# Kernel tuning notes

Hardware: AMD Instinct MI355X
Metric: run time of the kernel (lower is better)

The kernel has to match this reference:

```python
import jax, jax.numpy as jnp
import numpy as np

D_MODEL = 1024
NUM_HEADS = 16
HEAD_DIM = D_MODEL // NUM_HEADS


def setup_inputs() -> dict:
    key = jax.random.key(0)
    k_x, k_wqkv, k_bqkv, k_wo, k_bo = jax.random.split(key, 5)
    bound_qkv = 1.0 / np.sqrt(D_MODEL)
    x = jax.random.normal(k_x, (2, 2048, D_MODEL), dtype=jnp.float32)
    # torch nn.Linear init: U(-1/sqrt(fan_in), 1/sqrt(fan_in))
    W_qkv = jax.random.uniform(k_wqkv, (D_MODEL, 3 * D_MODEL), jnp.float32, -bound_qkv, bound_qkv)
    b_qkv = jax.random.uniform(k_bqkv, (3 * D_MODEL,), jnp.float32, -bound_qkv, bound_qkv)
    W_out = jax.random.uniform(k_wo, (D_MODEL, D_MODEL), jnp.float32, -bound_qkv, bound_qkv)
    b_out = jax.random.uniform(k_bo, (D_MODEL,), jnp.float32, -bound_qkv, bound_qkv)
    return {"x": x, "W_qkv": W_qkv, "b_qkv": b_qkv, "W_out": W_out, "b_out": b_out}


def reference(x, W_qkv, b_qkv, W_out, b_out):
    B, T, C = x.shape
    H, Dh = NUM_HEADS, HEAD_DIM
    qkv = x @ W_qkv + b_qkv                      # [B,T,3C]
    q, k, v = jnp.split(qkv, 3, axis=-1)
    # [B,T,C] -> [B,H,T,Dh]
    def to_heads(t):
        return t.reshape(B, T, H, Dh).transpose(0, 2, 1, 3)
    q, k, v = to_heads(q), to_heads(k), to_heads(v)
    scale = 1.0 / np.sqrt(Dh).astype(np.float32)
    scores = jnp.einsum("bhqd,bhkd->bhqk", q, k) * scale   # [B,H,T,T]
    weights = jax.nn.softmax(scores, axis=-1)
    attn = jnp.einsum("bhqk,bhkd->bhqd", weights, v)        # [B,H,T,Dh]
    attn = attn.transpose(0, 2, 1, 3).reshape(B, T, C)
    return attn @ W_out + b_out
```

## Files before the change

kernel.cpp:

```cpp
#include <hip/hip_runtime.h>

typedef __bf16 bf16x8 __attribute__((ext_vector_type(8)));
typedef float f32x4 __attribute__((ext_vector_type(4)));
typedef float f32x16 __attribute__((ext_vector_type(16)));

#define MFMA16(a, b, c) __builtin_amdgcn_mfma_f32_16x16x32_bf16(a, b, c, 0, 0, 0)
#define MFMA32(a, b, c) __builtin_amdgcn_mfma_f32_32x32x16_bf16(a, b, c, 0, 0, 0)
#define GLDS16(g, l)                                                              \
  __builtin_amdgcn_global_load_lds((const __attribute__((address_space(1))) void*)(g), \
                                   (__attribute__((address_space(3))) void*)(l), 16, 0, 0)

static __device__ __forceinline__ unsigned cvt_pk_bf16(float lo, float hi) {
  unsigned r;
  asm("v_cvt_pk_bf16_f32 %0, %1, %2" : "=v"(r) : "v"(lo), "v"(hi));
  return r;
}
static __device__ __forceinline__ void permswap(unsigned& a, unsigned& b) {
  asm("v_permlane32_swap_b32 %0, %1" : "+v"(a), "+v"(b));
}

__global__ __launch_bounds__(256) void cvt_bf16_kernel(const float* __restrict__ in,
                                                       __bf16* __restrict__ out, int n4) {
  int i = blockIdx.x * 256 + threadIdx.x;
  if (i < n4) {
    float4 v = ((const float4*)in)[i];
    union { __bf16 b[4]; uint2 u; } t;
    t.b[0] = (__bf16)v.x; t.b[1] = (__bf16)v.y;
    t.b[2] = (__bf16)v.z; t.b[3] = (__bf16)v.w;
    ((uint2*)out)[i] = t.u;
  }
}

__global__ __launch_bounds__(256) void transpose_w_kernel(const float* __restrict__ Wq,
                                                          __bf16* __restrict__ WqT,
                                                          const float* __restrict__ Wo,
                                                          __bf16* __restrict__ WoT) {
  const int Kd = 1024;
  int bx = blockIdx.x;
  const float* W; __bf16* WT; int Nd, n0;
  if (bx < 96) { W = Wq; WT = WqT; Nd = 3072; n0 = bx * 32; }
  else         { W = Wo; WT = WoT; Nd = 1024; n0 = (bx - 96) * 32; }
  __shared__ float tile[32][33];
  int k0 = blockIdx.y * 32;
  int tid = threadIdx.x;
  int kk = tid >> 3, nn = (tid & 7) * 4;
  float4 v = *(const float4*)&W[(size_t)(k0 + kk) * Nd + n0 + nn];
  tile[kk][nn] = v.x; tile[kk][nn + 1] = v.y;
  tile[kk][nn + 2] = v.z; tile[kk][nn + 3] = v.w;
  __syncthreads();
  int n2 = tid >> 3, k2 = (tid & 7) * 4;
  union { __bf16 b[4]; uint2 u; } t;
  t.b[0] = (__bf16)tile[k2][n2];
  t.b[1] = (__bf16)tile[k2 + 1][n2];
  t.b[2] = (__bf16)tile[k2 + 2][n2];
  t.b[3] = (__bf16)tile[k2 + 3][n2];
  *(uint2*)&WT[(size_t)(n0 + n2) * Kd + k0 + k2] = t.u;
}

template <bool OUT_F32, int NT>
__global__ __launch_bounds__(256) void gemm_kernel(const __bf16* __restrict__ A,
                                                   const __bf16* __restrict__ BT,
                                                   const float* __restrict__ bias,
                                                   void* __restrict__ Cout, int N,
                                                   int qn, float qs) {
  const int K = 1024;
  const int NJ = NT / 32;
  __shared__ __align__(16) __bf16 As[128 * 32];
  __shared__ __align__(16) __bf16 Bs[NT * 32];
  int tid = threadIdx.x;
  int wave = tid >> 6, lane = tid & 63;
  int quad = lane >> 4, l16 = lane & 15;
  int m0 = blockIdx.x * 128, n0 = blockIdx.y * NT;
  int wm = (wave >> 1) * 64, wn = (wave & 1) * (NT / 2);

  int srow = tid >> 2, scol = (tid & 3) * 8;
  const __bf16* aptr = A + (size_t)(m0 + srow) * K + scol;
  const __bf16* bptr = BT + (size_t)(n0 + srow) * K + scol;
  __bf16* asl = &As[(size_t)wave * 512];
  __bf16* bsl = &Bs[(size_t)wave * 512];

  f32x4 acc[4][NJ] = {};
  for (int k0 = 0; k0 < K; k0 += 32) {
    GLDS16(aptr + k0, asl);
    GLDS16(aptr + (size_t)64 * K + k0, asl + 2048);
    GLDS16(bptr + k0, bsl);
    if (NT == 128) GLDS16(bptr + (size_t)64 * K + k0, bsl + 2048);
    __syncthreads();
    bf16x8 af[4], bf[NJ];
    for (int i = 0; i < 4; i++)
      af[i] = *(bf16x8*)&As[(wm + i * 16 + l16) * 32 + quad * 8];
    for (int j = 0; j < NJ; j++)
      bf[j] = *(bf16x8*)&Bs[(wn + j * 16 + l16) * 32 + quad * 8];
    for (int i = 0; i < 4; i++)
      for (int j = 0; j < NJ; j++)
        acc[i][j] = MFMA16(af[i], bf[j], acc[i][j]);
    __syncthreads();
  }
  for (int j = 0; j < NJ; j++) {
    int col = n0 + wn + j * 16 + l16;
    float bv = bias[col];
    float sc = (col < qn) ? qs : 1.0f;
    for (int i = 0; i < 4; i++) {
      int rowb = m0 + wm + i * 16 + quad * 4;
      for (int r = 0; r < 4; r++) {
        float v = (acc[i][j][r] + bv) * sc;
        if (OUT_F32)
          ((float*)Cout)[(size_t)(rowb + r) * N + col] = v;
        else
          ((__bf16*)Cout)[(size_t)(rowb + r) * N + col] = (__bf16)v;
      }
    }
  }
}

__global__ __launch_bounds__(256) void transpose_v_kernel(const __bf16* __restrict__ qkv,
                                                          __bf16* __restrict__ Vt) {
  const int T = 2048, C3 = 3072;
  __shared__ __align__(16) __bf16 tile[64][72];
  int t0 = blockIdx.x * 64;
  int h = blockIdx.y, b = blockIdx.z;
  int tid = threadIdx.x;
  int tt = tid >> 2, c = (tid & 3) * 16;
  const __bf16* src = qkv + (size_t)(b * T + t0 + tt) * C3 + 2048 + h * 64 + c;
  *(uint4*)&tile[tt][c] = *(const uint4*)src;
  *(uint4*)&tile[tt][c + 8] = *(const uint4*)(src + 8);
  __syncthreads();
  int dd = tid >> 2, t2 = (tid & 3) * 16;
  union { __bf16 b_[16]; uint4 u[2]; } o;
  for (int i = 0; i < 16; i++) o.b_[i] = tile[t2 + i][dd];
  __bf16* dst = Vt + ((size_t)(b * 16 + h) * 64 + dd) * T + t0 + t2;
  *(uint4*)dst = o.u[0];
  *(uint4*)(dst + 8) = o.u[1];
}

struct AttnState {
  const char* lbase;
  char* wdst;
  int dK, dV;
  int lb[2][4];
};

template <int KRD, int VRD, int KST, int VST, bool DO_KST>
__device__ __forceinline__ void attn_iter(const AttnState& st, const __bf16* kg,
                                          const __bf16* vg, const bf16x8 (&qf)[4],
                                          const f32x16* sIN, f32x16* sOUT, f32x16& o0,
                                          f32x16& o1, float& rs) {
  __syncthreads();
  if constexpr (DO_KST) {
    GLDS16(kg, st.wdst + KST);
    GLDS16(kg + st.dK, st.wdst + KST + 4096);
  }
  GLDS16(vg, st.wdst + VST);
  GLDS16(vg + st.dV, st.wdst + VST + 4096);

  bf16x8 kf[2][4], vf[2][4];
#pragma unroll
  for (int rb = 0; rb < 2; rb++)
#pragma unroll
    for (int ds = 0; ds < 4; ds++)
      kf[rb][ds] = *(const bf16x8*)(st.lbase + st.lb[rb][ds] + KRD);
#pragma unroll
  for (int db = 0; db < 2; db++)
#pragma unroll
    for (int k2 = 0; k2 < 4; k2++)
      vf[db][k2] = *(const bf16x8*)(st.lbase + st.lb[db][k2] + VRD);

  f32x16 s0 = {}, s1 = {};
#pragma unroll
  for (int ds = 0; ds < 4; ds++) {
    s0 = MFMA32(kf[0][ds], qf[ds], s0);
    s1 = MFMA32(kf[1][ds], qf[ds], s1);
  }
  sOUT[0] = s0;
  sOUT[1] = s1;

  bf16x8 ap[4];
#pragma unroll
  for (int kb = 0; kb < 2; kb++) {
    float pv[16];
#pragma unroll
    for (int r = 0; r < 16; r++) {
      pv[r] = __builtin_amdgcn_exp2f(sIN[kb][r]);
      rs += pv[r];
    }
#pragma unroll
    for (int hf = 0; hf < 2; hf++) {
      unsigned w0 = cvt_pk_bf16(pv[hf * 8 + 0], pv[hf * 8 + 1]);
      unsigned w1 = cvt_pk_bf16(pv[hf * 8 + 2], pv[hf * 8 + 3]);
      unsigned w2 = cvt_pk_bf16(pv[hf * 8 + 4], pv[hf * 8 + 5]);
      unsigned w3 = cvt_pk_bf16(pv[hf * 8 + 6], pv[hf * 8 + 7]);
      permswap(w0, w2);
      permswap(w1, w3);
      union { unsigned u[4]; bf16x8 v; } pk;
      pk.u[0] = w0; pk.u[1] = w1; pk.u[2] = w2; pk.u[3] = w3;
      ap[kb * 2 + hf] = pk.v;
    }
  }

#pragma unroll
  for (int k2 = 0; k2 < 4; k2++) {
    o0 = MFMA32(ap[k2], vf[0][k2], o0);
    o1 = MFMA32(ap[k2], vf[1][k2], o1);
  }
}

__global__ __launch_bounds__(256, 2) void attn_kernel(const __bf16* __restrict__ qkv,
                                                      const __bf16* __restrict__ Vt,
                                                      __bf16* __restrict__ O) {
  const int T = 2048, C3 = 3072;
  int p = blockIdx.x * 4 + (blockIdx.y >> 4);
  int b = p >> 4, h = p & 15;
  int q0 = (blockIdx.y & 15) * 128;

  int tid = threadIdx.x, wave = tid >> 6, lane = tid & 63;
  int l32 = lane & 31, hi = lane >> 5;

  __shared__ __align__(16) __bf16 KV[4][64 * 64];

  const __bf16* qp = qkv + (size_t)(b * T + q0 + wave * 32 + l32) * C3 + h * 64;
  bf16x8 qf[4];
#pragma unroll
  for (int ds = 0; ds < 4; ds++)
    qf[ds] = *(const bf16x8*)(qp + ds * 16 + hi * 8);

  const __bf16* kbase = qkv + (size_t)(b * T) * C3 + 1024 + h * 64;
  const __bf16* vbase = Vt + (size_t)(b * 16 + h) * 64 * T;

  int srow = wave * 8 + (lane >> 3);
  int sx1 = ((lane & 7) ^ (lane >> 3) ^ wave) * 8;
  int sx2 = sx1 ^ 32;
  const __bf16* ksrc = kbase + (size_t)srow * C3 + sx1;
  const __bf16* vsrc = vbase + (size_t)srow * T + sx1;

  AttnState st;
  st.lbase = (const char*)&KV[0][0];
  st.wdst = (char*)&KV[0][0] + wave * 1024;
  st.dK = 32 * C3 + (sx2 - sx1);
  st.dV = 32 * T + (sx2 - sx1);
#pragma unroll
  for (int rb = 0; rb < 2; rb++)
#pragma unroll
    for (int c4 = 0; c4 < 4; c4++)
      st.lb[rb][c4] =
          ((rb * 32 + l32) * 64 +
           (((c4 * 2 + hi) ^ (l32 & 7) ^ (l32 >> 3) ^ (rb * 4)) * 8)) * 2;

  f32x16 o0 = {}, o1 = {};
  f32x16 sA[2], sB[2];
  float rs = 0.0f;

  GLDS16(ksrc, st.wdst + 0);
  GLDS16(ksrc + st.dK, st.wdst + 4096);
  GLDS16(vsrc, st.wdst + 8192);
  GLDS16(vsrc + st.dV, st.wdst + 8192 + 4096);
  GLDS16(ksrc + (size_t)64 * C3, st.wdst + 16384);
  GLDS16(ksrc + (size_t)64 * C3 + st.dK, st.wdst + 16384 + 4096);
  __syncthreads();

  {
    bf16x8 kf[2][4];
#pragma unroll
    for (int rb = 0; rb < 2; rb++)
#pragma unroll
      for (int ds = 0; ds < 4; ds++)
        kf[rb][ds] = *(const bf16x8*)(st.lbase + st.lb[rb][ds] + 0);
    f32x16 s0 = {}, s1 = {};
#pragma unroll
    for (int ds = 0; ds < 4; ds++) {
      s0 = MFMA32(kf[0][ds], qf[ds], s0);
      s1 = MFMA32(kf[1][ds], qf[ds], s1);
    }
    sA[0] = s0;
    sA[1] = s1;
  }

  const size_t kstep = (size_t)64 * C3;
  const __bf16* kg = ksrc + 2 * kstep;
  const __bf16* vg = vsrc + 64;

  for (int tp = 0; tp < 15; ++tp) {
    attn_iter<16384, 8192, 0, 24576, true>(st, kg, vg, qf, sA, sB, o0, o1, rs);
    kg += kstep; vg += 64;
    attn_iter<0, 24576, 16384, 8192, true>(st, kg, vg, qf, sB, sA, o0, o1, rs);
    kg += kstep; vg += 64;
  }
  attn_iter<16384, 8192, 0, 24576, false>(st, kg, vg, qf, sA, sB, o0, o1, rs);

  {
    __syncthreads();
    bf16x8 vf[2][4];
#pragma unroll
    for (int db = 0; db < 2; db++)
#pragma unroll
      for (int k2 = 0; k2 < 4; k2++)
        vf[db][k2] = *(const bf16x8*)(st.lbase + st.lb[db][k2] + 24576);
    bf16x8 ap[4];
#pragma unroll
    for (int kb = 0; kb < 2; kb++) {
      float pv[16];
#pragma unroll
      for (int r = 0; r < 16; r++) {
        pv[r] = __builtin_amdgcn_exp2f(sB[kb][r]);
        rs += pv[r];
      }
#pragma unroll
      for (int hf = 0; hf < 2; hf++) {
        unsigned w0 = cvt_pk_bf16(pv[hf * 8 + 0], pv[hf * 8 + 1]);
        unsigned w1 = cvt_pk_bf16(pv[hf * 8 + 2], pv[hf * 8 + 3]);
        unsigned w2 = cvt_pk_bf16(pv[hf * 8 + 4], pv[hf * 8 + 5]);
        unsigned w3 = cvt_pk_bf16(pv[hf * 8 + 6], pv[hf * 8 + 7]);
        permswap(w0, w2);
        permswap(w1, w3);
        union { unsigned u[4]; bf16x8 v; } pk;
        pk.u[0] = w0; pk.u[1] = w1; pk.u[2] = w2; pk.u[3] = w3;
        ap[kb * 2 + hf] = pk.v;
      }
    }
#pragma unroll
    for (int k2 = 0; k2 < 4; k2++) {
      o0 = MFMA32(ap[k2], vf[0][k2], o0);
      o1 = MFMA32(ap[k2], vf[1][k2], o1);
    }
  }

  unsigned xu = __float_as_uint(rs), yu = __float_as_uint(rs);
  permswap(xu, yu);
  float inv = 1.0f / (__uint_as_float(xu) + __uint_as_float(yu));
  float invv[16];
#pragma unroll
  for (int r = 0; r < 16; r++)
    invv[r] = __shfl(inv, (r & 3) + 8 * (r >> 2) + 4 * hi);

  __bf16* ob = O + (size_t)(b * T + q0 + wave * 32) * 1024 + h * 64 + l32;
#pragma unroll
  for (int r = 0; r < 16; r++) {
    int row = (r & 3) + 8 * (r >> 2) + 4 * hi;
    ob[(size_t)row * 1024] = (__bf16)(o0[r] * invv[r]);
    ob[(size_t)row * 1024 + 32] = (__bf16)(o1[r] * invv[r]);
  }
}

extern "C" void kernel_launch(void* const* d_in, const int* in_sizes, int n_in,
                              void* d_out, int out_size, void* d_ws, size_t ws_size,
                              hipStream_t stream) {
  const float* x = (const float*)d_in[0];
  const float* W_qkv = (const float*)d_in[1];
  const float* b_qkv = (const float*)d_in[2];
  const float* W_out = (const float*)d_in[3];
  const float* b_out = (const float*)d_in[4];
  float* out = (float*)d_out;

  char* ws = (char*)d_ws;
  __bf16* WqkvT = (__bf16*)(ws);
  __bf16* WoT = (__bf16*)(ws + 6291456);
  __bf16* xb = (__bf16*)(ws + 8388608);
  __bf16* qkvb = (__bf16*)(ws + 16777216);
  __bf16* Vt = (__bf16*)(ws + 41943040);
  __bf16* attnb = xb;

  const float cs = 0.125f * 1.44269504089f;

  cvt_bf16_kernel<<<4096, 256, 0, stream>>>(x, xb, 1048576);
  transpose_w_kernel<<<dim3(128, 32), 256, 0, stream>>>(W_qkv, WqkvT, W_out, WoT);
  gemm_kernel<false, 128><<<dim3(32, 24), 256, 0, stream>>>(xb, WqkvT, b_qkv, qkvb, 3072,
                                                            1024, cs);
  transpose_v_kernel<<<dim3(32, 16, 2), 256, 0, stream>>>(qkvb, Vt);
  attn_kernel<<<dim3(8, 64), 256, 0, stream>>>(qkvb, Vt, attnb);
  gemm_kernel<true, 64><<<dim3(32, 16), 256, 0, stream>>>(attnb, WoT, b_out, out, 1024,
                                                          0, 1.0f);
}
```

Measured before the change: 180.3 us.

## Merge input prep kernels and fuse V transpose into QKV GEMM epilogue

Combines the x-to-bf16 conversion and the weight transpose into a single prep kernel. It also removes the separate V transpose kernel by having the QKV GEMM epilogue write V columns straight into the transposed Vt layout. The aim is to cut two kernel launches and the extra read/write pass over V. The cost is scattered 2-byte stores into Vt from the GEMM epilogue, which coalesce poorly along T.

```diff
diff --git a/kernel.cpp b/kernel.cpp
--- a/kernel.cpp
+++ b/kernel.cpp
@@ -19,30 +19,31 @@
   asm("v_permlane32_swap_b32 %0, %1" : "+v"(a), "+v"(b));
 }
 
-__global__ __launch_bounds__(256) void cvt_bf16_kernel(const float* __restrict__ in,
-                                                       __bf16* __restrict__ out, int n4) {
-  int i = blockIdx.x * 256 + threadIdx.x;
-  if (i < n4) {
-    float4 v = ((const float4*)in)[i];
+__global__ __launch_bounds__(256) void prep_kernel(const float* __restrict__ x,
+                                                   __bf16* __restrict__ xb,
+                                                   const float* __restrict__ Wq,
+                                                   __bf16* __restrict__ WqT,
+                                                   const float* __restrict__ Wo,
+                                                   __bf16* __restrict__ WoT) {
+  __shared__ float tile[32][33];
+  int bid = blockIdx.x;
+  int tid = threadIdx.x;
+  if (bid < 4096) {
+    int i = bid * 256 + tid;
+    float4 v = ((const float4*)x)[i];
     union { __bf16 b[4]; uint2 u; } t;
     t.b[0] = (__bf16)v.x; t.b[1] = (__bf16)v.y;
     t.b[2] = (__bf16)v.z; t.b[3] = (__bf16)v.w;
-    ((uint2*)out)[i] = t.u;
-  }
-}
-
-__global__ __launch_bounds__(256) void transpose_w_kernel(const float* __restrict__ Wq,
-                                                          __bf16* __restrict__ WqT,
-                                                          const float* __restrict__ Wo,
-                                                          __bf16* __restrict__ WoT) {
+    ((uint2*)xb)[i] = t.u;
+    return;
+  }
   const int Kd = 1024;
-  int bx = blockIdx.x;
+  int b2 = bid - 4096;
+  int bx = b2 & 127;
+  int k0 = (b2 >> 7) * 32;
   const float* W; __bf16* WT; int Nd, n0;
   if (bx < 96) { W = Wq; WT = WqT; Nd = 3072; n0 = bx * 32; }
   else         { W = Wo; WT = WoT; Nd = 1024; n0 = (bx - 96) * 32; }
-  __shared__ float tile[32][33];
-  int k0 = blockIdx.y * 32;
-  int tid = threadIdx.x;
   int kk = tid >> 3, nn = (tid & 7) * 4;
   float4 v = *(const float4*)&W[(size_t)(k0 + kk) * Nd + n0 + nn];
   tile[kk][nn] = v.x; tile[kk][nn + 1] = v.y;
@@ -62,7 +63,8 @@
                                                    const __bf16* __restrict__ BT,
                                                    const float* __restrict__ bias,
                                                    void* __restrict__ Cout, int N,
-                                                   int qn, float qs) {
+                                                   int qn, float qs,
+                                                   __bf16* __restrict__ VtOut) {
   const int K = 1024;
   const int NJ = NT / 32;
   __shared__ __align__(16) __bf16 As[128 * 32];
@@ -96,10 +98,13 @@
         acc[i][j] = MFMA16(af[i], bf[j], acc[i][j]);
     __syncthreads();
   }
+  bool doV = (VtOut != nullptr) && (n0 >= 2048);
   for (int j = 0; j < NJ; j++) {
     int col = n0 + wn + j * 16 + l16;
     float bv = bias[col];
     float sc = (col < qn) ? qs : 1.0f;
+    int cc = col - 2048;
+    __bf16* vt = doV ? VtOut + ((size_t)(cc >> 6) * 64 + (cc & 63)) * 2048 : nullptr;
     for (int i = 0; i < 4; i++) {
       int rowb = m0 + wm + i * 16 + quad * 4;
       for (int r = 0; r < 4; r++) {
@@ -108,29 +113,13 @@
           ((float*)Cout)[(size_t)(rowb + r) * N + col] = v;
         else
           ((__bf16*)Cout)[(size_t)(rowb + r) * N + col] = (__bf16)v;
+        if (doV) {
+          int t_ = rowb + r;
+          vt[((size_t)(t_ >> 11) * 16 * 64) * 2048 + (t_ & 2047)] = (__bf16)v;
+        }
       }
     }
   }
-}
-
-__global__ __launch_bounds__(256) void transpose_v_kernel(const __bf16* __restrict__ qkv,
-                                                          __bf16* __restrict__ Vt) {
-  const int T = 2048, C3 = 3072;
-  __shared__ __align__(16) __bf16 tile[64][72];
-  int t0 = blockIdx.x * 64;
-  int h = blockIdx.y, b = blockIdx.z;
-  int tid = threadIdx.x;
-  int tt = tid >> 2, c = (tid & 3) * 16;
-  const __bf16* src = qkv + (size_t)(b * T + t0 + tt) * C3 + 2048 + h * 64 + c;
-  *(uint4*)&tile[tt][c] = *(const uint4*)src;
-  *(uint4*)&tile[tt][c + 8] = *(const uint4*)(src + 8);
-  __syncthreads();
-  int dd = tid >> 2, t2 = (tid & 3) * 16;
-  union { __bf16 b_[16]; uint4 u[2]; } o;
-  for (int i = 0; i < 16; i++) o.b_[i] = tile[t2 + i][dd];
-  __bf16* dst = Vt + ((size_t)(b * 16 + h) * 64 + dd) * T + t0 + t2;
-  *(uint4*)dst = o.u[0];
-  *(uint4*)(dst + 8) = o.u[1];
 }
 
 struct AttnState {
@@ -360,12 +349,10 @@
 
   const float cs = 0.125f * 1.44269504089f;
 
-  cvt_bf16_kernel<<<4096, 256, 0, stream>>>(x, xb, 1048576);
-  transpose_w_kernel<<<dim3(128, 32), 256, 0, stream>>>(W_qkv, WqkvT, W_out, WoT);
+  prep_kernel<<<8192, 256, 0, stream>>>(x, xb, W_qkv, WqkvT, W_out, WoT);
   gemm_kernel<false, 128><<<dim3(32, 24), 256, 0, stream>>>(xb, WqkvT, b_qkv, qkvb, 3072,
-                                                            1024, cs);
-  transpose_v_kernel<<<dim3(32, 16, 2), 256, 0, stream>>>(qkvb, Vt);
+                                                            1024, cs, Vt);
   attn_kernel<<<dim3(8, 64), 256, 0, stream>>>(qkvb, Vt, attnb);
   gemm_kernel<true, 64><<<dim3(32, 16), 256, 0, stream>>>(attnb, WoT, b_out, out, 1024,
-                                                          0, 1.0f);
-}
+                                                          0, 1.0f, nullptr);
+}
```

Result: slower. 197.9 us (+9.8%).
